# Optimization experiments

Hardware: AMD Instinct MI355X
Metric: run time of the kernel (lower is better)

Reference implementation:

```python
import jax, jax.numpy as jnp
import numpy as np

EPS = 1e-5
GROUPS = 32

def group_norm(x, gamma, beta):
    B, C, H, W = x.shape
    g = x.reshape(B, GROUPS, C // GROUPS, H, W)
    mu = g.mean(axis=(2, 3, 4), keepdims=True)
    var = g.var(axis=(2, 3, 4), keepdims=True)
    g = (g - mu) * jax.lax.rsqrt(var + EPS)
    x = g.reshape(B, C, H, W)
    return x * gamma[None, :, None, None] + beta[None, :, None, None]

def setup_inputs() -> dict:
    key = jax.random.key(0)
    ks = jax.random.split(key, 6)
    C = 512
    x = jax.random.normal(ks[0], (16, C, 32, 32), dtype=jnp.float32)
    gamma = jnp.ones((C,), jnp.float32)
    beta = jnp.zeros((C,), jnp.float32)
    w_qkv = jax.random.normal(ks[1], (3 * C, C), jnp.float32) / np.sqrt(C)
    b_qkv = jnp.zeros((3 * C,), jnp.float32)
    w_proj = jax.random.normal(ks[2], (C, C), jnp.float32) / np.sqrt(C)
    b_proj = jnp.zeros((C,), jnp.float32)
    return {"x": x, "gamma": gamma, "beta": beta, "w_qkv": w_qkv,
            "b_qkv": b_qkv, "w_proj": w_proj, "b_proj": b_proj}

def reference(x, gamma, beta, w_qkv, b_qkv, w_proj, b_proj):
    B, C, H, W = x.shape
    h = group_norm(x, gamma, beta)
    # 1x1 conv == per-pixel linear over channels
    qkv = jnp.einsum('bchw,oc->bohw', h, w_qkv) + b_qkv[None, :, None, None]
    q, k, v = jnp.split(qkv, 3, axis=1)
    N = H * W
    q = q.reshape(B, C, N)            # [B,C,N]
    k = k.reshape(B, C, N)
    v = v.reshape(B, C, N)
    attn = jnp.einsum('bci,bcj->bij', q, k) / jnp.sqrt(jnp.float32(C))
    attn = jax.nn.softmax(attn, axis=-1)          # [B,N,N]
    out = jnp.einsum('bij,bcj->bci', attn, v)     # [B,C,N]
    out = out.reshape(B, C, H, W)
    out = jnp.einsum('bchw,oc->bohw', out, w_proj) + b_proj[None, :, None, None]
    return x + out
```

## Files before the change

### kernel.cpp

```cpp
#include <hip/hip_runtime.h>
#include <hip/hip_bf16.h>

#define BATCH 16
#define CH    512
#define NPIX  1024
#define GRP   32
#define CPG   16

typedef __attribute__((ext_vector_type(8))) short bf16x8;
typedef __attribute__((ext_vector_type(4))) float f32x4;

__device__ __forceinline__ ushort f2b(float f) {
    union { float f; unsigned u; } v; v.f = f;
    unsigned u = v.u;
    u += 0x7FFF + ((u >> 16) & 1);
    return (ushort)(u >> 16);
}

#define GLD16(gp, lp) __builtin_amdgcn_global_load_lds( \
    (__attribute__((address_space(1))) void*)(gp), \
    (__attribute__((address_space(3))) void*)(lp), 16, 0, 0)

__global__ __launch_bounds__(256) void gn_fused(
    const float* __restrict__ x, const float* __restrict__ gamma,
    const float* __restrict__ beta, ushort* __restrict__ hT,
    const float* __restrict__ wq, const float* __restrict__ wp,
    ushort* __restrict__ wq_b, ushort* __restrict__ wp_b,
    float* __restrict__ rowsum) {
    __shared__ float xs[CPG * NPIX];
    __shared__ float as[4], bs[4];
    int g = blockIdx.x, b = blockIdx.y;

    {
        int bid = g + GRP * b;
        int base = bid * 2048 + threadIdx.x * 8;
        const float* srcp = (base < 786432) ? (wq + base) : (wp + (base - 786432));
        ushort*      dstp = (base < 786432) ? (wq_b + base) : (wp_b + (base - 786432));
        float4 a = *(const float4*)srcp;
        float4 c = *(const float4*)(srcp + 4);
        ushort t8[8] = {f2b(a.x), f2b(a.y), f2b(a.z), f2b(a.w),
                        f2b(c.x), f2b(c.y), f2b(c.z), f2b(c.w)};
        *(uint4*)dstp = *(const uint4*)t8;
        if (bid < 16) {
            float4 z = {0.f, 0.f, 0.f, 0.f};
            ((float4*)rowsum)[bid * 256 + threadIdx.x] = z;
        }
    }

    const float4* p = (const float4*)(x + ((size_t)b * CH + g * CPG) * NPIX);
    float4* xs4 = (float4*)xs;
    float s = 0.f, ss = 0.f;
    for (int i = threadIdx.x; i < 4096; i += 256) {
        float4 v = p[i];
        xs4[i] = v;
        s  += v.x + v.y + v.z + v.w;
        ss += v.x*v.x + v.y*v.y + v.z*v.z + v.w*v.w;
    }
    for (int o = 1; o < 64; o <<= 1) { s += __shfl_xor(s, o); ss += __shfl_xor(ss, o); }
    int w = threadIdx.x >> 6;
    if ((threadIdx.x & 63) == 0) { as[w] = s; bs[w] = ss; }
    __syncthreads();
    s  = as[0] + as[1] + as[2] + as[3];
    ss = bs[0] + bs[1] + bs[2] + bs[3];
    float m   = s * (1.0f / 16384.0f);
    float var = ss * (1.0f / 16384.0f) - m * m;
    float r   = rsqrtf(var + 1e-5f);

    int c0 = g * CPG;
    float ga[CPG], be[CPG];
#pragma unroll
    for (int c = 0; c < CPG; c++) {
        float gg = gamma[c0 + c] * r;
        ga[c] = gg;
        be[c] = beta[c0 + c] - m * gg;
    }
    ushort tmp[CPG];
#pragma unroll
    for (int i = 0; i < 4; i++) {
        int n = threadIdx.x + i * 256;
#pragma unroll
        for (int c = 0; c < CPG; c++)
            tmp[c] = f2b(xs[c * NPIX + n] * ga[c] + be[c]);
        uint4* dst = (uint4*)(hT + ((size_t)b * NPIX + n) * CH + c0);
        dst[0] = *(const uint4*)&tmp[0];
        dst[1] = *(const uint4*)&tmp[8];
    }
}

#define BK 64

template<int EPI, int BMt, int BNt>
__global__ __launch_bounds__(256, 4) void gemm_bt(
    const ushort* __restrict__ A, long sA, int lda,
    const ushort* __restrict__ Bt, long sB, int ldb,
    int K,
    void* __restrict__ Out, long sO, int ldo,
    const float* __restrict__ bias,
    const float* __restrict__ resid,
    ushort* __restrict__ vout,
    float* __restrict__ rowsum,
    float scale) {
    constexpr int FM = BMt / 32;
    constexpr int FN = BNt / 32;
    constexpr int SA = BMt / 32;
    constexpr int SB = BNt / 32;
    __shared__ __align__(16) ushort sh[(BMt + BNt) * BK];
    ushort* As = sh;
    ushort* Bs = sh + BMt * BK;

    int nx = gridDim.x, ny = gridDim.y;
    int L = blockIdx.x + nx * (blockIdx.y + ny * blockIdx.z);
    int per = (nx * ny * (int)gridDim.z) >> 3;
    int wid = (L & 7) * per + (L >> 3);
    int bx = wid % nx; wid /= nx;
    int by = wid % ny;
    int b  = wid / ny;

    A  += (size_t)b * sA;
    Bt += (size_t)b * sB;
    int m0 = by * BMt, n0 = bx * BNt;
    int tid = threadIdx.x;
    int lane = tid & 63;
    int wave = tid >> 6;
    int q = lane >> 4, l = lane & 15;
    int wm = (wave >> 1) * (BMt / 2), wn = (wave & 1) * (BNt / 2);

    int aoff[SA], boff[SB], lofa[SA], lofb[SB];
#pragma unroll
    for (int i = 0; i < SA; i++) {
        int p = tid + i * 256, r = p >> 3, g = (p & 7) ^ (r & 7);
        aoff[i] = (m0 + r) * lda + g * 8;
        lofa[i] = p * 8;
    }
#pragma unroll
    for (int i = 0; i < SB; i++) {
        int p = tid + i * 256, r = p >> 3, g = (p & 7) ^ (r & 7);
        boff[i] = (n0 + r) * ldb + g * 8;
        lofb[i] = p * 8;
    }

    int offA[FM][2], offB[FN][2];
#pragma unroll
    for (int mi = 0; mi < FM; mi++) {
        int r = wm + mi * 16 + l;
#pragma unroll
        for (int kk = 0; kk < 2; kk++)
            offA[mi][kk] = r * 64 + ((((kk << 2) | q) ^ (r & 7)) * 8);
    }
#pragma unroll
    for (int ni = 0; ni < FN; ni++) {
        int r = wn + ni * 16 + l;
#pragma unroll
        for (int kk = 0; kk < 2; kk++)
            offB[ni][kk] = r * 64 + ((((kk << 2) | q) ^ (r & 7)) * 8);
    }

    f32x4 zero = {0.f, 0.f, 0.f, 0.f};
    f32x4 acc[FM][FN];
#pragma unroll
    for (int mi = 0; mi < FM; mi++)
#pragma unroll
        for (int ni = 0; ni < FN; ni++) acc[mi][ni] = zero;

    for (int k0 = 0; k0 < K; k0 += BK) {
        __syncthreads();
#pragma unroll
        for (int i = 0; i < SA; i++) GLD16(A + aoff[i] + k0, As + lofa[i]);
#pragma unroll
        for (int i = 0; i < SB; i++) GLD16(Bt + boff[i] + k0, Bs + lofb[i]);
        __syncthreads();
#pragma unroll
        for (int kk = 0; kk < 2; kk++) {
            bf16x8 af[FM], bfr[FN];
#pragma unroll
            for (int mi = 0; mi < FM; mi++) af[mi]  = *(const bf16x8*)(As + offA[mi][kk]);
#pragma unroll
            for (int ni = 0; ni < FN; ni++) bfr[ni] = *(const bf16x8*)(Bs + offB[ni][kk]);
#pragma unroll
            for (int mi = 0; mi < FM; mi++)
#pragma unroll
                for (int ni = 0; ni < FN; ni++)
                    acc[mi][ni] = __builtin_amdgcn_mfma_f32_16x16x32_bf16(
                        af[mi], bfr[ni], acc[mi][ni], 0, 0, 0);
        }
    }

    if (EPI == 0) {
        if (n0 >= 1024) {
            __syncthreads();
#pragma unroll
            for (int mi = 0; mi < FM; mi++)
#pragma unroll
                for (int ni = 0; ni < FN; ni++) {
                    int nl = wn + ni * 16 + l;
                    float bi = bias[n0 + nl];
#pragma unroll
                    for (int rg = 0; rg < 4; rg++) {
                        int ml = wm + mi * 16 + q * 4 + rg;
                        int pos = (ml >> 3) ^ (nl & 15);
                        sh[nl * 128 + pos * 8 + (ml & 7)] = f2b(acc[mi][ni][rg] + bi);
                    }
                }
            __syncthreads();
#pragma unroll
            for (int i = 0; i < 8; i++) {
                int idx = tid + i * 256;
                int nl = idx >> 4, ch = idx & 15;
                int g2 = ch ^ (nl & 15);
                uint4 val = *(const uint4*)&sh[nl * 128 + g2 * 8];
                *(uint4*)(vout + (size_t)b * (512 * 1024)
                          + (size_t)(n0 - 1024 + nl) * 1024 + m0 + ch * 8) = val;
            }
            return;
        }
#pragma unroll
        for (int mi = 0; mi < FM; mi++)
#pragma unroll
            for (int ni = 0; ni < FN; ni++) {
                int n = n0 + wn + ni * 16 + l;
                float bi = bias[n];
#pragma unroll
                for (int rg = 0; rg < 4; rg++) {
                    int m = m0 + wm + mi * 16 + q * 4 + rg;
                    ((ushort*)Out)[(size_t)b * sO + (size_t)m * ldo + n] =
                        f2b(acc[mi][ni][rg] + bi);
                }
            }
        return;
    }
    if (EPI == 1) {
#pragma unroll
        for (int mi = 0; mi < FM; mi++) {
            float rsum[4] = {0.f, 0.f, 0.f, 0.f};
#pragma unroll
            for (int ni = 0; ni < FN; ni++) {
                int n = n0 + wn + ni * 16 + l;
#pragma unroll
                for (int rg = 0; rg < 4; rg++) {
                    int m = m0 + wm + mi * 16 + q * 4 + rg;
                    float u = __expf(acc[mi][ni][rg] * scale);
                    rsum[rg] += u;
                    ((ushort*)Out)[(size_t)b * sO + (size_t)m * ldo + n] = f2b(u);
                }
            }
#pragma unroll
            for (int rg = 0; rg < 4; rg++) {
                float s = rsum[rg];
                s += __shfl_xor(s, 1); s += __shfl_xor(s, 2);
                s += __shfl_xor(s, 4); s += __shfl_xor(s, 8);
                if (l == 0)
                    atomicAdd(&rowsum[b * NPIX + m0 + wm + mi * 16 + q * 4 + rg], s);
            }
        }
        return;
    }
#pragma unroll
    for (int mi = 0; mi < FM; mi++) {
        float inv[4];
        if (EPI == 2) {
#pragma unroll
            for (int rg = 0; rg < 4; rg++)
                inv[rg] = 1.0f / rowsum[b * NPIX + m0 + wm + mi * 16 + q * 4 + rg];
        }
#pragma unroll
        for (int ni = 0; ni < FN; ni++) {
            int mbase = m0 + wm + mi * 16 + q * 4;
            int n = n0 + wn + ni * 16 + l;
#pragma unroll
            for (int rg = 0; rg < 4; rg++) {
                int m = mbase + rg;
                float v = acc[mi][ni][rg];
                if (EPI == 2) {
                    ((ushort*)Out)[(size_t)b * sO + (size_t)m * ldo + n] = f2b(v * inv[rg]);
                } else {
                    v += bias[m] + resid[(size_t)b * sO + (size_t)m * ldo + n];
                    ((float*)Out)[(size_t)b * sO + (size_t)m * ldo + n] = v;
                }
            }
        }
    }
}

extern "C" void kernel_launch(void* const* d_in, const int* in_sizes, int n_in,
                              void* d_out, int out_size, void* d_ws, size_t ws_size,
                              hipStream_t stream) {
    const float* x     = (const float*)d_in[0];
    const float* gamma = (const float*)d_in[1];
    const float* beta  = (const float*)d_in[2];
    const float* wqkv  = (const float*)d_in[3];
    const float* bqkv  = (const float*)d_in[4];
    const float* wproj = (const float*)d_in[5];
    const float* bproj = (const float*)d_in[6];
    float* out = (float*)d_out;
    char* ws = (char*)d_ws;

    ushort* wq_b   = (ushort*)(ws + 0);
    ushort* wp_b   = (ushort*)(ws + 1572864);
    float*  rowsum = (float*)(ws + 2101248);
    ushort* hT     = (ushort*)(ws + 2166784);
    ushort* qk     = (ushort*)(ws + 18944000);
    ushort* vb     = (ushort*)(ws + 52498432);
    ushort* u      = (ushort*)(ws + 69275648);
    ushort* O1T    = hT;

    gn_fused<<<dim3(GRP, BATCH), 256, 0, stream>>>(
        x, gamma, beta, hT, wqkv, wproj, wq_b, wp_b, rowsum);

    gemm_bt<0, 128, 128><<<dim3(12, 8, BATCH), 256, 0, stream>>>(
        hT, 524288, 512, wq_b, 0, 512, 512,
        qk, 1048576, 1024, bqkv, nullptr, vb, nullptr, 0.f);

    gemm_bt<1, 128, 128><<<dim3(8, 8, BATCH), 256, 0, stream>>>(
        qk, 1048576, 1024, qk + 512, 1048576, 1024, 512,
        u, 1048576, 1024, nullptr, nullptr, nullptr, rowsum, 0.044194173824159216f);

    gemm_bt<2, 128, 64><<<dim3(8, 8, BATCH), 256, 0, stream>>>(
        u, 1048576, 1024, vb, 524288, 1024, 1024,
        O1T, 524288, 512, nullptr, nullptr, nullptr, rowsum, 0.f);

    gemm_bt<3, 64, 128><<<dim3(8, 8, BATCH), 256, 0, stream>>>(
        wp_b, 0, 512, O1T, 524288, 512, 512,
        out, 524288, 1024, bproj, x, nullptr, nullptr, 0.f);
}
```

Baseline: 208.0 us.

## Replace QK^T GEMM with dedicated 256x256-tile kernel using 512 threads

Adds a specialized mm2_qk kernel for the attention-score GEMM. It uses 256x256 tiles with 8 waves each computing 128x64, double-buffered LDS loads via global_load_lds, and an XOR-swizzled layout. It also remaps block IDs so that work is spread across XCDs and raises MFMA priority with setprio. The larger tiles should give more data reuse per byte loaded. The cost is only 256 blocks, which may leave CUs underfilled, plus high register pressure from 32 accumulators per thread.

```diff
diff --git a/kernel.cpp b/kernel.cpp
--- a/kernel.cpp
+++ b/kernel.cpp
@@ -228,32 +228,6 @@
             }
         return;
     }
-    if (EPI == 1) {
-#pragma unroll
-        for (int mi = 0; mi < FM; mi++) {
-            float rsum[4] = {0.f, 0.f, 0.f, 0.f};
-#pragma unroll
-            for (int ni = 0; ni < FN; ni++) {
-                int n = n0 + wn + ni * 16 + l;
-#pragma unroll
-                for (int rg = 0; rg < 4; rg++) {
-                    int m = m0 + wm + mi * 16 + q * 4 + rg;
-                    float u = __expf(acc[mi][ni][rg] * scale);
-                    rsum[rg] += u;
-                    ((ushort*)Out)[(size_t)b * sO + (size_t)m * ldo + n] = f2b(u);
-                }
-            }
-#pragma unroll
-            for (int rg = 0; rg < 4; rg++) {
-                float s = rsum[rg];
-                s += __shfl_xor(s, 1); s += __shfl_xor(s, 2);
-                s += __shfl_xor(s, 4); s += __shfl_xor(s, 8);
-                if (l == 0)
-                    atomicAdd(&rowsum[b * NPIX + m0 + wm + mi * 16 + q * 4 + rg], s);
-            }
-        }
-        return;
-    }
 #pragma unroll
     for (int mi = 0; mi < FM; mi++) {
         float inv[4];
@@ -277,6 +251,130 @@
                     ((float*)Out)[(size_t)b * sO + (size_t)m * ldo + n] = v;
                 }
             }
+        }
+    }
+}
+
+__global__ __launch_bounds__(512, 2) void mm2_qk(
+    const ushort* __restrict__ qk, ushort* __restrict__ u,
+    float* __restrict__ rowsum) {
+    constexpr int BM = 256, BN = 256;
+    constexpr int SA = 4, SB = 4;
+    constexpr int BUF = (BM + BN) * BK;
+    __shared__ __align__(16) ushort sh[2 * BUF];
+
+    int L = blockIdx.x + 4 * (blockIdx.y + 4 * blockIdx.z);
+    int wid = (L & 7) * 32 + (L >> 3);
+    int bx = wid & 3;
+    int by = (wid >> 2) & 3;
+    int b  = wid >> 4;
+
+    const ushort* A  = qk + (size_t)b * 1048576;
+    const ushort* Bt = A + 512;
+    int m0 = by * BM, n0 = bx * BN;
+    int tid = threadIdx.x;
+    int lane = tid & 63;
+    int wave = tid >> 6;
+    int q = lane >> 4, l = lane & 15;
+    int wm = (wave >> 2) * 128, wn = (wave & 3) * 64;
+
+    int aoff[SA], boff[SB], lof[SA];
+#pragma unroll
+    for (int i = 0; i < SA; i++) {
+        int p = tid + i * 512, r = p >> 3, g = (p & 7) ^ (r & 7);
+        aoff[i] = (m0 + r) * 1024 + g * 8;
+        boff[i] = (n0 + r) * 1024 + g * 8;
+        lof[i]  = p * 8;
+    }
+
+    int offA[8][2], offB[4][2];
+#pragma unroll
+    for (int mi = 0; mi < 8; mi++) {
+        int r = wm + mi * 16 + l;
+#pragma unroll
+        for (int kk = 0; kk < 2; kk++)
+            offA[mi][kk] = r * 64 + ((((kk << 2) | q) ^ (r & 7)) * 8);
+    }
+#pragma unroll
+    for (int ni = 0; ni < 4; ni++) {
+        int r = wn + ni * 16 + l;
+#pragma unroll
+        for (int kk = 0; kk < 2; kk++)
+            offB[ni][kk] = r * 64 + ((((kk << 2) | q) ^ (r & 7)) * 8);
+    }
+
+    f32x4 zero = {0.f, 0.f, 0.f, 0.f};
+    f32x4 acc[8][4];
+#pragma unroll
+    for (int mi = 0; mi < 8; mi++)
+#pragma unroll
+        for (int ni = 0; ni < 4; ni++) acc[mi][ni] = zero;
+
+#pragma unroll
+    for (int i = 0; i < SA; i++) GLD16(A + aoff[i], sh + lof[i]);
+#pragma unroll
+    for (int i = 0; i < SB; i++) GLD16(Bt + boff[i], sh + BM * BK + lof[i]);
+
+    for (int t = 0; t < 8; t++) {
+        const int cur = t & 1;
+        const ushort* Asc = sh + cur * BUF;
+        const ushort* Bsc = Asc + BM * BK;
+        if (t < 7) {
+            ushort* Asn = sh + (cur ^ 1) * BUF;
+            ushort* Bsn = Asn + BM * BK;
+            int k1 = (t + 1) * BK;
+#pragma unroll
+            for (int i = 0; i < SA; i++) GLD16(A + aoff[i] + k1, Asn + lof[i]);
+#pragma unroll
+            for (int i = 0; i < SB; i++) GLD16(Bt + boff[i] + k1, Bsn + lof[i]);
+            asm volatile("s_waitcnt vmcnt(%0)" :: "i"(SA + SB) : "memory");
+        } else {
+            asm volatile("s_waitcnt vmcnt(0)" ::: "memory");
+        }
+        __builtin_amdgcn_s_barrier();
+        __builtin_amdgcn_sched_barrier(0);
+#pragma unroll
+        for (int kk = 0; kk < 2; kk++) {
+            bf16x8 af[8], bfr[4];
+#pragma unroll
+            for (int mi = 0; mi < 8; mi++) af[mi]  = *(const bf16x8*)(Asc + offA[mi][kk]);
+#pragma unroll
+            for (int ni = 0; ni < 4; ni++) bfr[ni] = *(const bf16x8*)(Bsc + offB[ni][kk]);
+            __builtin_amdgcn_s_setprio(1);
+#pragma unroll
+            for (int mi = 0; mi < 8; mi++)
+#pragma unroll
+                for (int ni = 0; ni < 4; ni++)
+                    acc[mi][ni] = __builtin_amdgcn_mfma_f32_16x16x32_bf16(
+                        af[mi], bfr[ni], acc[mi][ni], 0, 0, 0);
+            __builtin_amdgcn_s_setprio(0);
+        }
+        __builtin_amdgcn_sched_barrier(0);
+        __builtin_amdgcn_s_barrier();
+    }
+
+    const float scale = 0.044194173824159216f;
+#pragma unroll
+    for (int mi = 0; mi < 8; mi++) {
+        float rsum4[4] = {0.f, 0.f, 0.f, 0.f};
+#pragma unroll
+        for (int ni = 0; ni < 4; ni++) {
+            int n = n0 + wn + ni * 16 + l;
+#pragma unroll
+            for (int rg = 0; rg < 4; rg++) {
+                int m = m0 + wm + mi * 16 + q * 4 + rg;
+                float uu = __expf(acc[mi][ni][rg] * scale);
+                rsum4[rg] += uu;
+                u[(size_t)b * 1048576 + (size_t)m * 1024 + n] = f2b(uu);
+            }
+        }
+#pragma unroll
+        for (int rg = 0; rg < 4; rg++) {
+            float s = rsum4[rg];
+            s += __shfl_xor(s, 1); s += __shfl_xor(s, 2);
+            s += __shfl_xor(s, 4); s += __shfl_xor(s, 8);
+            if (l == 0)
+                atomicAdd(&rowsum[b * NPIX + m0 + wm + mi * 16 + q * 4 + rg], s);
         }
     }
 }
@@ -310,9 +408,7 @@
         hT, 524288, 512, wq_b, 0, 512, 512,
         qk, 1048576, 1024, bqkv, nullptr, vb, nullptr, 0.f);
 
-    gemm_bt<1, 128, 128><<<dim3(8, 8, BATCH), 256, 0, stream>>>(
-        qk, 1048576, 1024, qk + 512, 1048576, 1024, 512,
-        u, 1048576, 1024, nullptr, nullptr, nullptr, rowsum, 0.044194173824159216f);
+    mm2_qk<<<dim3(4, 4, BATCH), 512, 0, stream>>>(qk, u, rowsum);
 
     gemm_bt<2, 128, 64><<<dim3(8, 8, BATCH), 256, 0, stream>>>(
         u, 1048576, 1024, vb, 524288, 1024, 1024,
```

After: 208.1 us. Within noise of the previous version (+0.0%).

## Double-buffer LDS tiles in the attention-times-V GEMM

Applied to the files above, without the earlier changes.

Adds a templated double-buffered K loop to the GEMM that prefetches the next K tile into a second LDS buffer while MFMAs consume the current one. It uses explicit vmcnt waits and raw barriers in place of two __syncthreads per iteration. Only the P·V GEMM (EPI 2, K=1024) enables it. This aims to hide global-to-LDS load latency, but doubles the shared memory per block, which can lower occupancy under the 4-blocks-per-CU launch bound.

```diff
diff --git a/kernel.cpp b/kernel.cpp
--- a/kernel.cpp
+++ b/kernel.cpp
@@ -89,7 +89,7 @@
 
 #define BK 64
 
-template<int EPI, int BMt, int BNt>
+template<int EPI, int BMt, int BNt, bool PIPE>
 __global__ __launch_bounds__(256, 4) void gemm_bt(
     const ushort* __restrict__ A, long sA, int lda,
     const ushort* __restrict__ Bt, long sB, int ldb,
@@ -104,7 +104,9 @@
     constexpr int FN = BNt / 32;
     constexpr int SA = BMt / 32;
     constexpr int SB = BNt / 32;
-    __shared__ __align__(16) ushort sh[(BMt + BNt) * BK];
+    constexpr int BUFSZ = (BMt + BNt) * BK;
+    constexpr int NB = PIPE ? 2 : 1;
+    __shared__ __align__(16) ushort sh[NB * BUFSZ];
     ushort* As = sh;
     ushort* Bs = sh + BMt * BK;
 
@@ -162,26 +164,69 @@
 #pragma unroll
         for (int ni = 0; ni < FN; ni++) acc[mi][ni] = zero;
 
-    for (int k0 = 0; k0 < K; k0 += BK) {
-        __syncthreads();
-#pragma unroll
-        for (int i = 0; i < SA; i++) GLD16(A + aoff[i] + k0, As + lofa[i]);
-#pragma unroll
-        for (int i = 0; i < SB; i++) GLD16(Bt + boff[i] + k0, Bs + lofb[i]);
-        __syncthreads();
-#pragma unroll
-        for (int kk = 0; kk < 2; kk++) {
-            bf16x8 af[FM], bfr[FN];
-#pragma unroll
-            for (int mi = 0; mi < FM; mi++) af[mi]  = *(const bf16x8*)(As + offA[mi][kk]);
-#pragma unroll
-            for (int ni = 0; ni < FN; ni++) bfr[ni] = *(const bf16x8*)(Bs + offB[ni][kk]);
-#pragma unroll
-            for (int mi = 0; mi < FM; mi++)
-#pragma unroll
-                for (int ni = 0; ni < FN; ni++)
-                    acc[mi][ni] = __builtin_amdgcn_mfma_f32_16x16x32_bf16(
-                        af[mi], bfr[ni], acc[mi][ni], 0, 0, 0);
+    if constexpr (PIPE) {
+#pragma unroll
+        for (int i = 0; i < SA; i++) GLD16(A + aoff[i], sh + lofa[i]);
+#pragma unroll
+        for (int i = 0; i < SB; i++) GLD16(Bt + boff[i], sh + BMt * BK + lofb[i]);
+        const int nt = K / BK;
+        for (int t = 0; t < nt; t++) {
+            const int cur = t & 1;
+            const ushort* Asc = sh + cur * BUFSZ;
+            const ushort* Bsc = Asc + BMt * BK;
+            if (t + 1 < nt) {
+                ushort* Asn = sh + (cur ^ 1) * BUFSZ;
+                ushort* Bsn = Asn + BMt * BK;
+                int k1 = (t + 1) * BK;
+#pragma unroll
+                for (int i = 0; i < SA; i++) GLD16(A + aoff[i] + k1, Asn + lofa[i]);
+#pragma unroll
+                for (int i = 0; i < SB; i++) GLD16(Bt + boff[i] + k1, Bsn + lofb[i]);
+                asm volatile("s_waitcnt vmcnt(%0)" :: "i"(SA + SB) : "memory");
+            } else {
+                asm volatile("s_waitcnt vmcnt(0)" ::: "memory");
+            }
+            __builtin_amdgcn_s_barrier();
+            __builtin_amdgcn_sched_barrier(0);
+#pragma unroll
+            for (int kk = 0; kk < 2; kk++) {
+                bf16x8 af[FM], bfr[FN];
+#pragma unroll
+                for (int mi = 0; mi < FM; mi++) af[mi]  = *(const bf16x8*)(Asc + offA[mi][kk]);
+#pragma unroll
+                for (int ni = 0; ni < FN; ni++) bfr[ni] = *(const bf16x8*)(Bsc + offB[ni][kk]);
+#pragma unroll
+                for (int mi = 0; mi < FM; mi++)
+#pragma unroll
+                    for (int ni = 0; ni < FN; ni++)
+                        acc[mi][ni] = __builtin_amdgcn_mfma_f32_16x16x32_bf16(
+                            af[mi], bfr[ni], acc[mi][ni], 0, 0, 0);
+            }
+            __builtin_amdgcn_sched_barrier(0);
+            __builtin_amdgcn_s_barrier();
+        }
+    } else {
+        for (int k0 = 0; k0 < K; k0 += BK) {
+            __syncthreads();
+#pragma unroll
+            for (int i = 0; i < SA; i++) GLD16(A + aoff[i] + k0, As + lofa[i]);
+#pragma unroll
+            for (int i = 0; i < SB; i++) GLD16(Bt + boff[i] + k0, Bs + lofb[i]);
+            __syncthreads();
+#pragma unroll
+            for (int kk = 0; kk < 2; kk++) {
+                bf16x8 af[FM], bfr[FN];
+#pragma unroll
+                for (int mi = 0; mi < FM; mi++) af[mi]  = *(const bf16x8*)(As + offA[mi][kk]);
+#pragma unroll
+                for (int ni = 0; ni < FN; ni++) bfr[ni] = *(const bf16x8*)(Bs + offB[ni][kk]);
+#pragma unroll
+                for (int mi = 0; mi < FM; mi++)
+#pragma unroll
+                    for (int ni = 0; ni < FN; ni++)
+                        acc[mi][ni] = __builtin_amdgcn_mfma_f32_16x16x32_bf16(
+                            af[mi], bfr[ni], acc[mi][ni], 0, 0, 0);
+            }
         }
     }
 
@@ -306,19 +351,19 @@
     gn_fused<<<dim3(GRP, BATCH), 256, 0, stream>>>(
         x, gamma, beta, hT, wqkv, wproj, wq_b, wp_b, rowsum);
 
-    gemm_bt<0, 128, 128><<<dim3(12, 8, BATCH), 256, 0, stream>>>(
+    gemm_bt<0, 128, 128, false><<<dim3(12, 8, BATCH), 256, 0, stream>>>(
         hT, 524288, 512, wq_b, 0, 512, 512,
         qk, 1048576, 1024, bqkv, nullptr, vb, nullptr, 0.f);
 
-    gemm_bt<1, 128, 128><<<dim3(8, 8, BATCH), 256, 0, stream>>>(
+    gemm_bt<1, 128, 128, false><<<dim3(8, 8, BATCH), 256, 0, stream>>>(
         qk, 1048576, 1024, qk + 512, 1048576, 1024, 512,
         u, 1048576, 1024, nullptr, nullptr, nullptr, rowsum, 0.044194173824159216f);
 
-    gemm_bt<2, 128, 64><<<dim3(8, 8, BATCH), 256, 0, stream>>>(
+    gemm_bt<2, 128, 64, true><<<dim3(8, 8, BATCH), 256, 0, stream>>>(
         u, 1048576, 1024, vb, 524288, 1024, 1024,
         O1T, 524288, 512, nullptr, nullptr, nullptr, rowsum, 0.f);
 
-    gemm_bt<3, 64, 128><<<dim3(8, 8, BATCH), 256, 0, stream>>>(
+    gemm_bt<3, 64, 128, false><<<dim3(8, 8, BATCH), 256, 0, stream>>>(
         wp_b, 0, 512, O1T, 524288, 512, 512,
         out, 524288, 1024, bproj, x, nullptr, nullptr, 0.f);
 }
```

New measurement: 211.9 us. About the same (+1.9%).
